# Performance work log

Measured on AMD Instinct MI355X. Metric: run time of the kernel, lower is better.

The kernel has to match this reference:

```python
import jax, jax.numpy as jnp
import numpy as np
import math

# Model hyperparameters (SchNet defaults)
H = 128        # hidden_channels
F = 128        # num_filters
G = 50         # num_gaussians
CUT = 6.0      # cutoff (Angstrom)
L_INT = 3      # num_interactions
# Graph scale
N_MOL = 512    # molecules
APM = 32       # atoms per molecule
N = N_MOL * APM
BOX = 10.0     # side of cubic box per molecule


def _ssp(x):
    # ShiftedSoftplus
    return jax.nn.softplus(x) - math.log(2.0)


def setup_inputs() -> dict:
    rng = np.random.default_rng(0)
    pos = rng.uniform(0.0, BOX, (N_MOL, APM, 3)).astype(np.float32)
    # radius graph within each molecule (faithful to radius_graph_custom,
    # precomputed here because edge count is data-dependent)
    srcs, dsts = [], []
    for m in range(N_MOL):
        p = pos[m]
        dm = np.linalg.norm(p[:, None, :] - p[None, :, :], axis=-1)
        mask = dm <= CUT
        np.fill_diagonal(mask, False)
        s, t = np.nonzero(mask)
        srcs.append(s + m * APM)
        dsts.append(t + m * APM)
    edge_index = np.stack([np.concatenate(srcs), np.concatenate(dsts)]).astype(np.int32)
    pos = pos.reshape(N, 3)
    batch = np.repeat(np.arange(N_MOL, dtype=np.int32), APM)
    z = rng.integers(1, 100, N).astype(np.int32)

    key = jax.random.key(0)
    ks = jax.random.split(key, 16)
    s = 0.1
    nrm = lambda k, shp: (jax.random.normal(k, shp, dtype=jnp.float32) * s)
    return {
        "z": jnp.asarray(z),
        "pos": jnp.asarray(pos),
        "batch": jnp.asarray(batch),
        "edge_index": jnp.asarray(edge_index),
        "emb": nrm(ks[0], (100, H)),
        "mlp_w1": nrm(ks[1], (L_INT, G, F)),
        "mlp_b1": jnp.zeros((L_INT, F), jnp.float32),
        "mlp_w2": nrm(ks[2], (L_INT, F, F)),
        "mlp_b2": jnp.zeros((L_INT, F), jnp.float32),
        "cf1_w": nrm(ks[3], (L_INT, H, F)),
        "cf2_w": nrm(ks[4], (L_INT, F, H)),
        "cf2_b": jnp.zeros((L_INT, H), jnp.float32),
        "lin_w": nrm(ks[5], (L_INT, H, H)),
        "lin_b": jnp.zeros((L_INT, H), jnp.float32),
        "out1_w": nrm(ks[6], (H, H // 2)),
        "out1_b": jnp.zeros((H // 2,), jnp.float32),
        "out2_w": nrm(ks[7], (H // 2, 1)),
        "out2_b": jnp.zeros((1,), jnp.float32),
    }


def reference(z, pos, batch, edge_index, emb,
              mlp_w1, mlp_b1, mlp_w2, mlp_b2,
              cf1_w, cf2_w, cf2_b, lin_w, lin_b,
              out1_w, out1_b, out2_w, out2_b):
    src, dst = edge_index[0], edge_index[1]
    # edge_weight = euclidean distance (== cdist[src, dst])
    d = jnp.sqrt(jnp.sum((pos[src] - pos[dst]) ** 2, axis=-1))  # [E]
    # GaussianSmearing
    offs = jnp.linspace(0.0, CUT, G)
    coeff = -0.5 / (CUT / (G - 1)) ** 2
    edge_attr = jnp.exp(coeff * (d[:, None] - offs[None, :]) ** 2)  # [E, G]
    # cosine cutoff
    Ccut = 0.5 * (jnp.cos(d * math.pi / CUT) + 1.0)  # [E]

    h = emb[z]  # [N, H]
    for l in range(L_INT):
        # edge filter MLP with cutoff
        W = _ssp(edge_attr @ mlp_w1[l] + mlp_b1[l]) @ mlp_w2[l] + mlp_b2[l]  # [E, F]
        W = W * Ccut[:, None]
        # CFConv: lin1 -> gather x_j -> multiply -> scatter-add to dst -> lin2
        msg = (h @ cf1_w[l])[src] * W                                # [E, F]
        agg = jax.ops.segment_sum(msg, dst, num_segments=N)          # [N, F]
        v = agg @ cf2_w[l] + cf2_b[l]                                # [N, H]
        v = _ssp(v)
        v = v @ lin_w[l] + lin_b[l]
        h = h + v  # residual

    h = _ssp(h @ out1_w + out1_b)
    h = h @ out2_w + out2_b                                          # [N, 1]
    out = jax.ops.segment_sum(h, batch, num_segments=N_MOL)          # [N_MOL, 1]
    return out
```

## Files before the change

kernel.cpp:

```cpp
#include <hip/hip_runtime.h>
#include <hip/hip_bf16.h>
#include <math.h>

#define NATOMS 16384
#define NMOL   512
#define APM    32
#define GDIM   50
#define KTAB   2048
#define MAXEPM 992

#define STRH 132
#define STRA 136

typedef __attribute__((ext_vector_type(8))) short   short8;
typedef __attribute__((ext_vector_type(4))) float   floatx4;

__device__ __forceinline__ float ssp(float x) {
    float e = __expf(-fabsf(x));
    return fmaxf(x, 0.0f) + __logf(1.0f + e) - 0.69314718055994531f;
}

__device__ __forceinline__ unsigned short f2bf(float x) {
    union { float f; unsigned int u; } v; v.f = x;
    unsigned int lsb = (v.u >> 16) & 1u;
    v.u += 0x7fffu + lsb;
    return (unsigned short)(v.u >> 16);
}

__device__ __forceinline__ unsigned int pk2bf(float a, float b) {
    __hip_bfloat162 h = __float22bfloat162_rn(make_float2(a, b));
    unsigned int u;
    __builtin_memcpy(&u, &h, 4);
    return u;
}

__global__ __launch_bounds__(256) void setup_kernel(
    const float* __restrict__ pos, const int* __restrict__ eidx, int E,
    int* __restrict__ rowptr,
    const float* __restrict__ cf1, const float* __restrict__ cf2,
    const float* __restrict__ lin, const float* __restrict__ out1,
    unsigned short* __restrict__ Wtall, uint2* __restrict__ meta)
{
    int idx = blockIdx.x * 256 + threadIdx.x;
    if (idx < E) {
        int s = eidx[idx], t = eidx[E + idx];
        float dx = pos[3 * s]     - pos[3 * t];
        float dy = pos[3 * s + 1] - pos[3 * t + 1];
        float dz = pos[3 * s + 2] - pos[3 * t + 2];
        float d  = sqrtf(dx * dx + dy * dy + dz * dz);
        float u  = d * (float)(KTAB - 1) / 6.0f;
        int i = min((int)u, KTAB - 2);
        float frac = u - (float)i;
        meta[idx] = make_uint2(((unsigned)i << 5) | (unsigned)(t & 31),
                               __float_as_uint(frac));
    } else if (idx < E + NATOMS + 1) {
        int a = idx - E;
        int lo = 0, hi = E;
        while (lo < hi) { int mid = (lo + hi) >> 1; if (eidx[mid] < a) lo = mid + 1; else hi = mid; }
        rowptr[a] = lo;
    } else if (idx < E + NATOMS + 1 + 9 * 16384 + 64 * 128) {
        int r = idx - (E + NATOMS + 1);
        if (r < 9 * 16384) {
            int wi = r >> 14, rem = r & 16383;
            int n = rem >> 7, k = rem & 127;
            int l = wi / 3, which = wi % 3;
            const float* src = (which == 0) ? cf1 : (which == 1) ? cf2 : lin;
            Wtall[r] = f2bf(src[(size_t)l * 16384 + k * 128 + n]);
        } else {
            int q = r - 9 * 16384;
            int n = q >> 7, k = q & 127;
            Wtall[r] = f2bf(out1[k * 64 + n]);
        }
    }
}

#define KW1 72
#define KW2 136

__global__ __launch_bounds__(256, 2) void build_table_kernel(
    const float* __restrict__ w1_, const float* __restrict__ b1_,
    const float* __restrict__ w2_, const float* __restrict__ b2_,
    unsigned short* __restrict__ T_)
{
    const int l = blockIdx.y;
    const float* w1 = w1_ + (size_t)l * GDIM * 128;
    const float* b1 = b1_ + (size_t)l * 128;
    const float* w2 = w2_ + (size_t)l * 128 * 128;
    const float* b2 = b2_ + (size_t)l * 128;
    unsigned short* T = T_ + (size_t)l * KTAB * 128;

    __shared__ unsigned short s_w1T[128 * KW1];
    __shared__ unsigned short s_w2T[128 * KW2];
    __shared__ unsigned short s_t[64 * KW2];

    const int tid = threadIdx.x;
    for (int i = tid; i < GDIM * 128; i += 256) {
        int g = i >> 7, f = i & 127;
        s_w1T[f * KW1 + g] = f2bf(w1[i]);
    }
    for (int i = tid; i < (64 - GDIM) * 128; i += 256) {
        int g = GDIM + (i >> 7), f = i & 127;
        s_w1T[f * KW1 + g] = 0;
    }
    for (int i = tid; i < 128 * 128; i += 256) {
        int k = i >> 7, n = i & 127;
        s_w2T[n * KW2 + k] = f2bf(w2[i]);
    }

    const int lane = tid & 63;
    const int w    = tid >> 6;
    const int l15  = lane & 15;
    const int quad = lane >> 4;

    float b1v[8], b2v[8];
    #pragma unroll
    for (int nt = 0; nt < 8; nt++) {
        b1v[nt] = b1[nt * 16 + l15];
        b2v[nt] = b2[nt * 16 + l15];
    }
    __syncthreads();

    const float hstep = 6.0f / (float)(KTAB - 1);
    const float step  = 6.0f / 49.0f;
    const float coeff = -0.5f / (step * step);
    const float pioc  = 3.14159265358979323846f / 6.0f;
    const int k0 = blockIdx.x * 64;
    const float dm = (float)(k0 + w * 16 + l15) * hstep;

    floatx4 acc1[8];
    #pragma unroll
    for (int nt = 0; nt < 8; nt++) acc1[nt] = (floatx4){0.f, 0.f, 0.f, 0.f};
    #pragma unroll
    for (int ks = 0; ks < 2; ks++) {
        unsigned int ap[4];
        #pragma unroll
        for (int jj = 0; jj < 4; jj++) {
            int g0 = ks * 32 + quad * 8 + 2 * jj;
            float d0 = dm - (float)g0 * step;
            float d1 = dm - (float)(g0 + 1) * step;
            float v0 = (g0 < GDIM)     ? __expf(coeff * d0 * d0) : 0.0f;
            float v1 = (g0 + 1 < GDIM) ? __expf(coeff * d1 * d1) : 0.0f;
            ap[jj] = pk2bf(v0, v1);
        }
        short8 af;
        __builtin_memcpy(&af, ap, 16);
        #pragma unroll
        for (int nt = 0; nt < 8; nt++) {
            short8 bfg = *(const short8*)&s_w1T[(nt * 16 + l15) * KW1 + ks * 32 + quad * 8];
            acc1[nt] = __builtin_amdgcn_mfma_f32_16x16x32_bf16(af, bfg, acc1[nt], 0, 0, 0);
        }
    }
    #pragma unroll
    for (int nt = 0; nt < 8; nt++) {
        #pragma unroll
        for (int r = 0; r < 4; r++) {
            int row = w * 16 + quad * 4 + r;
            s_t[row * KW2 + nt * 16 + l15] = f2bf(ssp(acc1[nt][r] + b1v[nt]));
        }
    }

    floatx4 acc2[8];
    #pragma unroll
    for (int nt = 0; nt < 8; nt++) acc2[nt] = (floatx4){0.f, 0.f, 0.f, 0.f};
    #pragma unroll
    for (int ks = 0; ks < 4; ks++) {
        short8 af = *(const short8*)&s_t[(w * 16 + l15) * KW2 + ks * 32 + quad * 8];
        #pragma unroll
        for (int nt = 0; nt < 8; nt++) {
            short8 bfg = *(const short8*)&s_w2T[(nt * 16 + l15) * KW2 + ks * 32 + quad * 8];
            acc2[nt] = __builtin_amdgcn_mfma_f32_16x16x32_bf16(af, bfg, acc2[nt], 0, 0, 0);
        }
    }

    #pragma unroll
    for (int nt = 0; nt < 8; nt++) {
        #pragma unroll
        for (int r = 0; r < 4; r++) {
            int row = w * 16 + quad * 4 + r;
            float d = (float)(k0 + row) * hstep;
            float cut = 0.5f * (__cosf(d * pioc) + 1.0f);
            T[(size_t)(k0 + row) * 128 + nt * 16 + l15] = f2bf((acc2[nt][r] + b2v[nt]) * cut);
        }
    }
}

__global__ __launch_bounds__(256) void pack_table_kernel(
    const unsigned short* __restrict__ T, unsigned int* __restrict__ Tp)
{
    int idx = blockIdx.x * 256 + threadIdx.x;
    int k = (idx >> 7) & (KTAB - 1);
    unsigned int w0 = T[idx];
    float w0f = __uint_as_float(w0 << 16);
    float w1f = (k == KTAB - 1) ? w0f
              : __uint_as_float((unsigned int)T[idx + 128] << 16);
    unsigned int dw = f2bf(w1f - w0f);
    Tp[idx] = w0 | (dw << 16);
}

__global__ __launch_bounds__(512) void fused_schnet_kernel(
    const int* __restrict__ z, const float* __restrict__ emb,
    const int* __restrict__ rowptr, const uint2* __restrict__ meta,
    const unsigned int* __restrict__ Tp,
    const unsigned short* __restrict__ Wtall,
    const float* __restrict__ cf2_b, const float* __restrict__ lin_b,
    const float* __restrict__ out1_b, const float* __restrict__ out2_w,
    const float* __restrict__ out2_b,
    float* __restrict__ out)
{
    __shared__ float s_h[32 * STRH];
    __shared__ float s_hx[32 * 128];
    __shared__ unsigned short s_agg[32 * STRA];
    __shared__ uint2 s_meta[MAXEPM];
    __shared__ float s_red;
    unsigned short* s_t = (unsigned short*)s_hx;

    const int tid  = threadIdx.x;
    const int lane = tid & 63;
    const int w    = tid >> 6;
    const int l15  = lane & 15;
    const int quad = lane >> 4;
    const int r16  = (w & 1) * 16;
    const int c32  = (w >> 1) * 32;
    const int B0   = blockIdx.x * 32;

    for (int i = tid; i < 32 * 128; i += 512) {
        int row = i >> 7, col = i & 127;
        s_h[row * STRH + col] = emb[(size_t)z[B0 + row] * 128 + col];
    }
    if (tid == 0) s_red = 0.0f;

    const int ebase = rowptr[B0];
    const int nE    = rowptr[B0 + 32] - ebase;
    for (int i = tid; i < nE; i += 512) s_meta[i] = meta[ebase + i];

    const int rp = rowptr[B0 + w * 4 + min(lane, 4)] - ebase;

    const unsigned short* WtO = Wtall + 9 * 16384;

    for (int l = 0; l < 3; l++) {
        const unsigned short* W1 = Wtall + (size_t)(l * 3 + 0) * 16384;
        const unsigned short* W2 = Wtall + (size_t)(l * 3 + 1) * 16384;
        const unsigned short* W3 = Wtall + (size_t)(l * 3 + 2) * 16384;
        const unsigned int* Tpl  = Tp + (size_t)l * KTAB * 128;

        __syncthreads();

        floatx4 acc[2];
        #pragma unroll
        for (int nt = 0; nt < 2; nt++) acc[nt] = (floatx4){0.f, 0.f, 0.f, 0.f};
        #pragma unroll
        for (int ks = 0; ks < 4; ks++) {
            const float* hp = &s_h[(r16 + l15) * STRH + ks * 32 + quad * 8];
            float4 xa = *(const float4*)hp;
            float4 xb = *(const float4*)(hp + 4);
            unsigned int ap[4];
            ap[0] = pk2bf(xa.x, xa.y); ap[1] = pk2bf(xa.z, xa.w);
            ap[2] = pk2bf(xb.x, xb.y); ap[3] = pk2bf(xb.z, xb.w);
            short8 af;
            __builtin_memcpy(&af, ap, 16);
            #pragma unroll
            for (int nt = 0; nt < 2; nt++) {
                short8 bfg = *(const short8*)&W1[(size_t)(c32 + nt * 16 + l15) * 128 + ks * 32 + quad * 8];
                acc[nt] = __builtin_amdgcn_mfma_f32_16x16x32_bf16(af, bfg, acc[nt], 0, 0, 0);
            }
        }
        #pragma unroll
        for (int nt = 0; nt < 2; nt++) {
            #pragma unroll
            for (int r = 0; r < 4; r++)
                s_hx[(r16 + quad * 4 + r) * 128 + c32 + nt * 16 + l15] = acc[nt][r];
        }

        __syncthreads();

        for (int al = 0; al < 4; al++) {
            const int e0 = __shfl(rp, al);
            const int e1 = __shfl(rp, al + 1);
            float ax[8], ay[8];
            #pragma unroll
            for (int j = 0; j < 8; j++) { ax[j] = 0.f; ay[j] = 0.f; }
            int e = e0;
            for (; e + 7 < e1; e += 8) {
                #pragma unroll
                for (int j = 0; j < 8; j++) {
                    uint2 q = s_meta[e + j];
                    int tl   = q.x & 31;
                    int knot = q.x >> 5;
                    uint2 tp = *(const uint2*)&Tpl[(size_t)knot * 128 + 2 * lane];
                    float2 hv = *(const float2*)&s_hx[tl * 128 + 2 * lane];
                    float fr = __uint_as_float(q.y);
                    float wx = fmaf(fr, __uint_as_float(tp.x & 0xffff0000u),
                                    __uint_as_float(tp.x << 16));
                    float wy = fmaf(fr, __uint_as_float(tp.y & 0xffff0000u),
                                    __uint_as_float(tp.y << 16));
                    ax[j] = fmaf(hv.x, wx, ax[j]);
                    ay[j] = fmaf(hv.y, wy, ay[j]);
                }
            }
            for (; e < e1; e++) {
                int j = (e - e0) & 7;
                uint2 q = s_meta[e];
                int tl   = q.x & 31;
                int knot = q.x >> 5;
                uint2 tp = *(const uint2*)&Tpl[(size_t)knot * 128 + 2 * lane];
                float2 hv = *(const float2*)&s_hx[tl * 128 + 2 * lane];
                float fr = __uint_as_float(q.y);
                float wx = fmaf(fr, __uint_as_float(tp.x & 0xffff0000u),
                                __uint_as_float(tp.x << 16));
                float wy = fmaf(fr, __uint_as_float(tp.y & 0xffff0000u),
                                __uint_as_float(tp.y << 16));
                ax[j] = fmaf(hv.x, wx, ax[j]);
                ay[j] = fmaf(hv.y, wy, ay[j]);
            }
            float sx = ((ax[0] + ax[1]) + (ax[2] + ax[3])) + ((ax[4] + ax[5]) + (ax[6] + ax[7]));
            float sy = ((ay[0] + ay[1]) + (ay[2] + ay[3])) + ((ay[4] + ay[5]) + (ay[6] + ay[7]));
            *(unsigned int*)&s_agg[(w * 4 + al) * STRA + 2 * lane] = pk2bf(sx, sy);
        }

        __syncthreads();

        float bva[2], bvb[2];
        #pragma unroll
        for (int nt = 0; nt < 2; nt++) {
            bva[nt] = cf2_b[l * 128 + c32 + nt * 16 + l15];
            bvb[nt] = lin_b[l * 128 + c32 + nt * 16 + l15];
        }
        #pragma unroll
        for (int nt = 0; nt < 2; nt++) acc[nt] = (floatx4){0.f, 0.f, 0.f, 0.f};
        #pragma unroll
        for (int ks = 0; ks < 4; ks++) {
            short8 af = *(const short8*)&s_agg[(r16 + l15) * STRA + ks * 32 + quad * 8];
            #pragma unroll
            for (int nt = 0; nt < 2; nt++) {
                short8 bfg = *(const short8*)&W2[(size_t)(c32 + nt * 16 + l15) * 128 + ks * 32 + quad * 8];
                acc[nt] = __builtin_amdgcn_mfma_f32_16x16x32_bf16(af, bfg, acc[nt], 0, 0, 0);
            }
        }
        #pragma unroll
        for (int nt = 0; nt < 2; nt++) {
            #pragma unroll
            for (int r = 0; r < 4; r++) {
                int row = r16 + quad * 4 + r;
                s_t[row * STRA + c32 + nt * 16 + l15] = f2bf(ssp(acc[nt][r] + bva[nt]));
            }
        }

        __syncthreads();

        #pragma unroll
        for (int nt = 0; nt < 2; nt++) acc[nt] = (floatx4){0.f, 0.f, 0.f, 0.f};
        #pragma unroll
        for (int ks = 0; ks < 4; ks++) {
            short8 af = *(const short8*)&s_t[(r16 + l15) * STRA + ks * 32 + quad * 8];
            #pragma unroll
            for (int nt = 0; nt < 2; nt++) {
                short8 bfg = *(const short8*)&W3[(size_t)(c32 + nt * 16 + l15) * 128 + ks * 32 + quad * 8];
                acc[nt] = __builtin_amdgcn_mfma_f32_16x16x32_bf16(af, bfg, acc[nt], 0, 0, 0);
            }
        }
        #pragma unroll
        for (int nt = 0; nt < 2; nt++) {
            #pragma unroll
            for (int r = 0; r < 4; r++) {
                int row = r16 + quad * 4 + r;
                s_h[row * STRH + c32 + nt * 16 + l15] += acc[nt][r] + bvb[nt];
            }
        }
    }

    __syncthreads();

    const int c16 = (w >> 1) * 16;
    floatx4 ha = (floatx4){0.f, 0.f, 0.f, 0.f};
    #pragma unroll
    for (int ks = 0; ks < 4; ks++) {
        const float* hp = &s_h[(r16 + l15) * STRH + ks * 32 + quad * 8];
        float4 xa = *(const float4*)hp;
        float4 xb = *(const float4*)(hp + 4);
        unsigned int ap[4];
        ap[0] = pk2bf(xa.x, xa.y); ap[1] = pk2bf(xa.z, xa.w);
        ap[2] = pk2bf(xb.x, xb.y); ap[3] = pk2bf(xb.z, xb.w);
        short8 af;
        __builtin_memcpy(&af, ap, 16);
        short8 bfg = *(const short8*)&WtO[(size_t)(c16 + l15) * 128 + ks * 32 + quad * 8];
        ha = __builtin_amdgcn_mfma_f32_16x16x32_bf16(af, bfg, ha, 0, 0, 0);
    }
    float part = 0.0f;
    {
        float b1o = out1_b[c16 + l15];
        float o2  = out2_w[c16 + l15];
        #pragma unroll
        for (int r = 0; r < 4; r++)
            part += ssp(ha[r] + b1o) * o2;
    }
    #pragma unroll
    for (int off = 32; off > 0; off >>= 1) part += __shfl_down(part, off);
    if (lane == 0) atomicAdd(&s_red, part);
    __syncthreads();
    if (tid == 0) out[blockIdx.x] = s_red + 32.0f * out2_b[0];
}

extern "C" void kernel_launch(void* const* d_in, const int* in_sizes, int n_in,
                              void* d_out, int out_size, void* d_ws, size_t ws_size,
                              hipStream_t stream)
{
    const int*   z      = (const int*)d_in[0];
    const float* pos    = (const float*)d_in[1];
    const int*   eidx   = (const int*)d_in[3];
    const float* emb    = (const float*)d_in[4];
    const float* mlp_w1 = (const float*)d_in[5];
    const float* mlp_b1 = (const float*)d_in[6];
    const float* mlp_w2 = (const float*)d_in[7];
    const float* mlp_b2 = (const float*)d_in[8];
    const float* cf1_w  = (const float*)d_in[9];
    const float* cf2_w  = (const float*)d_in[10];
    const float* cf2_b  = (const float*)d_in[11];
    const float* lin_w  = (const float*)d_in[12];
    const float* lin_b  = (const float*)d_in[13];
    const float* out1_w = (const float*)d_in[14];
    const float* out1_b = (const float*)d_in[15];
    const float* out2_w = (const float*)d_in[16];
    const float* out2_b = (const float*)d_in[17];
    const int E = in_sizes[3] / 2;

    char* p = (char*)d_ws;
    uint2* meta = (uint2*)p;                      p += ((size_t)E * 8 + 63) & ~63ULL;
    unsigned int* Tp = (unsigned int*)p;          p += (size_t)3 * KTAB * 128 * 4;
    int* rowptr = (int*)p;                        p += ((size_t)(NATOMS + 1) * 4 + 63) & ~63ULL;
    unsigned short* Ttab = (unsigned short*)p;    p += (size_t)3 * KTAB * 128 * 2;
    unsigned short* Wtall = (unsigned short*)p;

    const int setup_work = E + (NATOMS + 1) + 9 * 16384 + 64 * 128;
    setup_kernel<<<(setup_work + 255) / 256, 256, 0, stream>>>(
        pos, eidx, E, rowptr, cf1_w, cf2_w, lin_w, out1_w, Wtall, meta);
    build_table_kernel<<<dim3(KTAB / 64, 3), 256, 0, stream>>>(
        mlp_w1, mlp_b1, mlp_w2, mlp_b2, Ttab);
    pack_table_kernel<<<3 * KTAB * 128 / 256, 256, 0, stream>>>(Ttab, Tp);

    fused_schnet_kernel<<<NMOL, 512, 0, stream>>>(
        z, emb, rowptr, meta, Tp, Wtall,
        cf2_b, lin_b, out1_b, out2_w, out2_b, (float*)d_out);
}
```

Before: 187.4 us.

## Exploit edge symmetry: process each undirected edge once with LDS atomic scatter

Setup now keeps only edges with t > s, compacting them per molecule into a padded list with a ballot-based wave compaction, so the CSR rowptr build is no longer needed. The fused kernel processes each undirected pair once: one filter-table lookup serves both directions, and the result is scattered to both endpoint rows through LDS float atomics into an fp32 aggregate buffer. This halves the filter-table gathers and the interpolation work. In exchange it adds four shared-memory atomics per edge per lane, zeroes the aggregate buffer every layer, and converts it to bf16 before the MFMA. It also assumes the input graph is symmetric, which holds for a radius graph.

```diff
diff --git a/kernel.cpp b/kernel.cpp
--- a/kernel.cpp
+++ b/kernel.cpp
@@ -7,7 +7,7 @@
 #define APM    32
 #define GDIM   50
 #define KTAB   2048
-#define MAXEPM 992
+#define MAXU   512
 
 #define STRH 132
 #define STRA 136
@@ -36,41 +36,65 @@
 
 __global__ __launch_bounds__(256) void setup_kernel(
     const float* __restrict__ pos, const int* __restrict__ eidx, int E,
-    int* __restrict__ rowptr,
     const float* __restrict__ cf1, const float* __restrict__ cf2,
     const float* __restrict__ lin, const float* __restrict__ out1,
-    unsigned short* __restrict__ Wtall, uint2* __restrict__ meta)
+    unsigned short* __restrict__ Wtall, uint2* __restrict__ umeta,
+    int* __restrict__ ucnt)
 {
-    int idx = blockIdx.x * 256 + threadIdx.x;
-    if (idx < E) {
-        int s = eidx[idx], t = eidx[E + idx];
-        float dx = pos[3 * s]     - pos[3 * t];
-        float dy = pos[3 * s + 1] - pos[3 * t + 1];
-        float dz = pos[3 * s + 2] - pos[3 * t + 2];
-        float d  = sqrtf(dx * dx + dy * dy + dz * dz);
-        float u  = d * (float)(KTAB - 1) / 6.0f;
-        int i = min((int)u, KTAB - 2);
-        float frac = u - (float)i;
-        meta[idx] = make_uint2(((unsigned)i << 5) | (unsigned)(t & 31),
-                               __float_as_uint(frac));
-    } else if (idx < E + NATOMS + 1) {
-        int a = idx - E;
+    if (blockIdx.x < NMOL) {
+        const int lane = threadIdx.x;
+        if (lane >= 64) return;
+        const int m  = blockIdx.x;
+        const int B0 = m * 32;
         int lo = 0, hi = E;
-        while (lo < hi) { int mid = (lo + hi) >> 1; if (eidx[mid] < a) lo = mid + 1; else hi = mid; }
-        rowptr[a] = lo;
-    } else if (idx < E + NATOMS + 1 + 9 * 16384 + 64 * 128) {
-        int r = idx - (E + NATOMS + 1);
-        if (r < 9 * 16384) {
-            int wi = r >> 14, rem = r & 16383;
-            int n = rem >> 7, k = rem & 127;
-            int l = wi / 3, which = wi % 3;
-            const float* src = (which == 0) ? cf1 : (which == 1) ? cf2 : lin;
-            Wtall[r] = f2bf(src[(size_t)l * 16384 + k * 128 + n]);
-        } else {
-            int q = r - 9 * 16384;
-            int n = q >> 7, k = q & 127;
-            Wtall[r] = f2bf(out1[k * 64 + n]);
-        }
+        while (lo < hi) { int mid = (lo + hi) >> 1; if (eidx[mid] < B0) lo = mid + 1; else hi = mid; }
+        const int e0 = lo; hi = E;
+        while (lo < hi) { int mid = (lo + hi) >> 1; if (eidx[mid] < B0 + 32) lo = mid + 1; else hi = mid; }
+        const int e1 = lo;
+
+        uint2* out = umeta + (size_t)m * MAXU;
+        int cnt = 0;
+        for (int base = e0; base < e1; base += 64) {
+            int e = base + lane;
+            bool keep = false;
+            uint2 val;
+            if (e < e1) {
+                int s = eidx[e], t = eidx[E + e];
+                if (t > s) {
+                    float dx = pos[3 * s]     - pos[3 * t];
+                    float dy = pos[3 * s + 1] - pos[3 * t + 1];
+                    float dz = pos[3 * s + 2] - pos[3 * t + 2];
+                    float d  = sqrtf(dx * dx + dy * dy + dz * dz);
+                    float u  = d * (float)(KTAB - 1) / 6.0f;
+                    int i = min((int)u, KTAB - 2);
+                    val = make_uint2(((unsigned)i << 12) |
+                                     ((unsigned)(s - B0) << 6) | (unsigned)(t - B0),
+                                     __float_as_uint(u - (float)i));
+                    keep = true;
+                }
+            }
+            unsigned long long mask = __ballot(keep);
+            int slot = __popcll(mask & ((1ULL << lane) - 1ULL));
+            if (keep) out[cnt + slot] = val;
+            cnt += (int)__popcll(mask);
+        }
+        int padded = (cnt + 63) & ~63;
+        for (int e = cnt + lane; e < padded; e += 64)
+            out[e] = make_uint2((32u << 6) | 32u, 0u);
+        if (lane == 0) ucnt[m] = padded;
+        return;
+    }
+    int idx = (blockIdx.x - NMOL) * 256 + threadIdx.x;
+    if (idx < 9 * 16384) {
+        int wi = idx >> 14, rem = idx & 16383;
+        int n = rem >> 7, k = rem & 127;
+        int l = wi / 3, which = wi % 3;
+        const float* src = (which == 0) ? cf1 : (which == 1) ? cf2 : lin;
+        Wtall[idx] = f2bf(src[(size_t)l * 16384 + k * 128 + n]);
+    } else if (idx < 9 * 16384 + 64 * 128) {
+        int q = idx - 9 * 16384;
+        int n = q >> 7, k = q & 127;
+        Wtall[idx] = f2bf(out1[k * 64 + n]);
     }
 }
 
@@ -199,7 +223,7 @@
 
 __global__ __launch_bounds__(512) void fused_schnet_kernel(
     const int* __restrict__ z, const float* __restrict__ emb,
-    const int* __restrict__ rowptr, const uint2* __restrict__ meta,
+    const uint2* __restrict__ umeta, const int* __restrict__ ucnt,
     const unsigned int* __restrict__ Tp,
     const unsigned short* __restrict__ Wtall,
     const float* __restrict__ cf2_b, const float* __restrict__ lin_b,
@@ -208,12 +232,11 @@
     float* __restrict__ out)
 {
     __shared__ float s_h[32 * STRH];
-    __shared__ float s_hx[32 * 128];
-    __shared__ unsigned short s_agg[32 * STRA];
-    __shared__ uint2 s_meta[MAXEPM];
+    __shared__ float s_hx[33 * 128];
+    __shared__ float s_agg[33 * STRH];
+    __shared__ uint2 s_meta[MAXU];
     __shared__ float s_red;
     unsigned short* s_t = (unsigned short*)s_hx;
-
     const int tid  = threadIdx.x;
     const int lane = tid & 63;
     const int w    = tid >> 6;
@@ -227,13 +250,11 @@
         int row = i >> 7, col = i & 127;
         s_h[row * STRH + col] = emb[(size_t)z[B0 + row] * 128 + col];
     }
+    if (tid < 128) s_hx[32 * 128 + tid] = 0.0f;
     if (tid == 0) s_red = 0.0f;
 
-    const int ebase = rowptr[B0];
-    const int nE    = rowptr[B0 + 32] - ebase;
-    for (int i = tid; i < nE; i += 512) s_meta[i] = meta[ebase + i];
-
-    const int rp = rowptr[B0 + w * 4 + min(lane, 4)] - ebase;
+    const int nU = ucnt[blockIdx.x];
+    for (int i = tid; i < nU; i += 512) s_meta[i] = umeta[(size_t)blockIdx.x * MAXU + i];
 
     const unsigned short* WtO = Wtall + 9 * 16384;
 
@@ -244,6 +265,8 @@
         const unsigned int* Tpl  = Tp + (size_t)l * KTAB * 128;
 
         __syncthreads();
+
+        for (int i = tid; i < 32 * STRH; i += 512) s_agg[i] = 0.0f;
 
         floatx4 acc[2];
         #pragma unroll
@@ -273,48 +296,26 @@
 
         __syncthreads();
 
-        for (int al = 0; al < 4; al++) {
-            const int e0 = __shfl(rp, al);
-            const int e1 = __shfl(rp, al + 1);
-            float ax[8], ay[8];
-            #pragma unroll
-            for (int j = 0; j < 8; j++) { ax[j] = 0.f; ay[j] = 0.f; }
-            int e = e0;
-            for (; e + 7 < e1; e += 8) {
-                #pragma unroll
-                for (int j = 0; j < 8; j++) {
-                    uint2 q = s_meta[e + j];
-                    int tl   = q.x & 31;
-                    int knot = q.x >> 5;
-                    uint2 tp = *(const uint2*)&Tpl[(size_t)knot * 128 + 2 * lane];
-                    float2 hv = *(const float2*)&s_hx[tl * 128 + 2 * lane];
-                    float fr = __uint_as_float(q.y);
-                    float wx = fmaf(fr, __uint_as_float(tp.x & 0xffff0000u),
-                                    __uint_as_float(tp.x << 16));
-                    float wy = fmaf(fr, __uint_as_float(tp.y & 0xffff0000u),
-                                    __uint_as_float(tp.y << 16));
-                    ax[j] = fmaf(hv.x, wx, ax[j]);
-                    ay[j] = fmaf(hv.y, wy, ay[j]);
-                }
-            }
-            for (; e < e1; e++) {
-                int j = (e - e0) & 7;
-                uint2 q = s_meta[e];
-                int tl   = q.x & 31;
-                int knot = q.x >> 5;
+        for (int base = w * 8; base < nU; base += 64) {
+            #pragma unroll
+            for (int j = 0; j < 8; j++) {
+                uint2 q = s_meta[base + j];
+                int b    = q.x & 63;
+                int a    = (q.x >> 6) & 63;
+                int knot = q.x >> 12;
                 uint2 tp = *(const uint2*)&Tpl[(size_t)knot * 128 + 2 * lane];
-                float2 hv = *(const float2*)&s_hx[tl * 128 + 2 * lane];
+                float2 hva = *(const float2*)&s_hx[a * 128 + 2 * lane];
+                float2 hvb = *(const float2*)&s_hx[b * 128 + 2 * lane];
                 float fr = __uint_as_float(q.y);
                 float wx = fmaf(fr, __uint_as_float(tp.x & 0xffff0000u),
                                 __uint_as_float(tp.x << 16));
                 float wy = fmaf(fr, __uint_as_float(tp.y & 0xffff0000u),
                                 __uint_as_float(tp.y << 16));
-                ax[j] = fmaf(hv.x, wx, ax[j]);
-                ay[j] = fmaf(hv.y, wy, ay[j]);
-            }
-            float sx = ((ax[0] + ax[1]) + (ax[2] + ax[3])) + ((ax[4] + ax[5]) + (ax[6] + ax[7]));
-            float sy = ((ay[0] + ay[1]) + (ay[2] + ay[3])) + ((ay[4] + ay[5]) + (ay[6] + ay[7]));
-            *(unsigned int*)&s_agg[(w * 4 + al) * STRA + 2 * lane] = pk2bf(sx, sy);
+                atomicAdd(&s_agg[a * STRH + 2 * lane],     hvb.x * wx);
+                atomicAdd(&s_agg[a * STRH + 2 * lane + 1], hvb.y * wy);
+                atomicAdd(&s_agg[b * STRH + 2 * lane],     hva.x * wx);
+                atomicAdd(&s_agg[b * STRH + 2 * lane + 1], hva.y * wy);
+            }
         }
 
         __syncthreads();
@@ -329,7 +330,14 @@
         for (int nt = 0; nt < 2; nt++) acc[nt] = (floatx4){0.f, 0.f, 0.f, 0.f};
         #pragma unroll
         for (int ks = 0; ks < 4; ks++) {
-            short8 af = *(const short8*)&s_agg[(r16 + l15) * STRA + ks * 32 + quad * 8];
+            const float* apf = &s_agg[(r16 + l15) * STRH + ks * 32 + quad * 8];
+            float4 xa = *(const float4*)apf;
+            float4 xb = *(const float4*)(apf + 4);
+            unsigned int ap[4];
+            ap[0] = pk2bf(xa.x, xa.y); ap[1] = pk2bf(xa.z, xa.w);
+            ap[2] = pk2bf(xb.x, xb.y); ap[3] = pk2bf(xb.z, xb.w);
+            short8 af;
+            __builtin_memcpy(&af, ap, 16);
             #pragma unroll
             for (int nt = 0; nt < 2; nt++) {
                 short8 bfg = *(const short8*)&W2[(size_t)(c32 + nt * 16 + l15) * 128 + ks * 32 + quad * 8];
@@ -424,20 +432,20 @@
     const int E = in_sizes[3] / 2;
 
     char* p = (char*)d_ws;
-    uint2* meta = (uint2*)p;                      p += ((size_t)E * 8 + 63) & ~63ULL;
+    uint2* umeta = (uint2*)p;                     p += (size_t)NMOL * MAXU * 8;
     unsigned int* Tp = (unsigned int*)p;          p += (size_t)3 * KTAB * 128 * 4;
-    int* rowptr = (int*)p;                        p += ((size_t)(NATOMS + 1) * 4 + 63) & ~63ULL;
+    int* ucnt = (int*)p;                          p += ((size_t)NMOL * 4 + 63) & ~63ULL;
     unsigned short* Ttab = (unsigned short*)p;    p += (size_t)3 * KTAB * 128 * 2;
     unsigned short* Wtall = (unsigned short*)p;
 
-    const int setup_work = E + (NATOMS + 1) + 9 * 16384 + 64 * 128;
-    setup_kernel<<<(setup_work + 255) / 256, 256, 0, stream>>>(
-        pos, eidx, E, rowptr, cf1_w, cf2_w, lin_w, out1_w, Wtall, meta);
+    const int wblocks = (9 * 16384 + 64 * 128 + 255) / 256;
+    setup_kernel<<<NMOL + wblocks, 256, 0, stream>>>(
+        pos, eidx, E, cf1_w, cf2_w, lin_w, out1_w, Wtall, umeta, ucnt);
     build_table_kernel<<<dim3(KTAB / 64, 3), 256, 0, stream>>>(
         mlp_w1, mlp_b1, mlp_w2, mlp_b2, Ttab);
     pack_table_kernel<<<3 * KTAB * 128 / 256, 256, 0, stream>>>(Ttab, Tp);
 
     fused_schnet_kernel<<<NMOL, 512, 0, stream>>>(
-        z, emb, rowptr, meta, Tp, Wtall,
+        z, emb, umeta, ucnt, Tp, Wtall,
         cf2_b, lin_b, out1_b, out2_w, out2_b, (float*)d_out);
 }
```

New measurement: 710.7 us. +279.3%, slower.

## Merge setup, table build and pack into one kernel; widen edge gather loop

Applied to the files above, without the earlier changes.

The three preprocessing kernels (edge metadata and rowptr, weight conversion, filter-table build plus delta packing) are combined into one launch. The table build now emits packed value/delta pairs straight from LDS in overlapping 63-row tiles, which removes the intermediate bf16 table and the separate pack pass. In the main kernel the edge aggregation has each half-wave handle alternate edges with 4 channels per lane and 128-bit loads. The loop is padded with a sentinel edge that points at a zeroed h row, so the scalar tail loop goes away, and the two half-wave partials are combined with a cross-lane shuffle. This adds a 4-wave occupancy hint and some padded-edge work in return for fewer launches and wider memory accesses.

```diff
diff --git a/kernel.cpp b/kernel.cpp
--- a/kernel.cpp
+++ b/kernel.cpp
@@ -7,7 +7,7 @@
 #define APM    32
 #define GDIM   50
 #define KTAB   2048
-#define MAXEPM 992
+#define MAXEPM 1000
 
 #define STRH 132
 #define STRA 136
@@ -27,6 +27,11 @@
     return (unsigned short)(v.u >> 16);
 }
 
+__device__ __forceinline__ float bf2f(unsigned int u16bits) {
+    union { unsigned int u; float f; } v; v.u = u16bits << 16;
+    return v.f;
+}
+
 __device__ __forceinline__ unsigned int pk2bf(float a, float b) {
     __hip_bfloat162 h = __float22bfloat162_rn(make_float2(a, b));
     unsigned int u;
@@ -34,66 +39,78 @@
     return u;
 }
 
-__global__ __launch_bounds__(256) void setup_kernel(
-    const float* __restrict__ pos, const int* __restrict__ eidx, int E,
+#define KW1 72
+#define KW2 136
+#define TILE_K 63
+#define NTILE 33
+
+__global__ __launch_bounds__(256) void mega_setup_kernel(
+    const float* __restrict__ pos, const int* __restrict__ eidx, int E, int EB,
     int* __restrict__ rowptr,
     const float* __restrict__ cf1, const float* __restrict__ cf2,
     const float* __restrict__ lin, const float* __restrict__ out1,
-    unsigned short* __restrict__ Wtall, uint2* __restrict__ meta)
+    unsigned short* __restrict__ Wtall, uint2* __restrict__ meta,
+    const float* __restrict__ w1_, const float* __restrict__ b1_,
+    const float* __restrict__ w2_, const float* __restrict__ b2_,
+    unsigned int* __restrict__ Tp)
 {
-    int idx = blockIdx.x * 256 + threadIdx.x;
-    if (idx < E) {
-        int s = eidx[idx], t = eidx[E + idx];
-        float dx = pos[3 * s]     - pos[3 * t];
-        float dy = pos[3 * s + 1] - pos[3 * t + 1];
-        float dz = pos[3 * s + 2] - pos[3 * t + 2];
-        float d  = sqrtf(dx * dx + dy * dy + dz * dz);
-        float u  = d * (float)(KTAB - 1) / 6.0f;
-        int i = min((int)u, KTAB - 2);
-        float frac = u - (float)i;
-        meta[idx] = make_uint2(((unsigned)i << 5) | (unsigned)(t & 31),
-                               __float_as_uint(frac));
-    } else if (idx < E + NATOMS + 1) {
-        int a = idx - E;
-        int lo = 0, hi = E;
-        while (lo < hi) { int mid = (lo + hi) >> 1; if (eidx[mid] < a) lo = mid + 1; else hi = mid; }
-        rowptr[a] = lo;
-    } else if (idx < E + NATOMS + 1 + 9 * 16384 + 64 * 128) {
-        int r = idx - (E + NATOMS + 1);
-        if (r < 9 * 16384) {
-            int wi = r >> 14, rem = r & 16383;
+    const int WB = (9 * 16384 + 64 * 128 + 255) / 256;
+    const int b = blockIdx.x;
+    const int tid = threadIdx.x;
+
+    if (b < EB) {
+        int idx = b * 256 + tid;
+        if (idx < E) {
+            int s = eidx[idx], t = eidx[E + idx];
+            float dx = pos[3 * s]     - pos[3 * t];
+            float dy = pos[3 * s + 1] - pos[3 * t + 1];
+            float dz = pos[3 * s + 2] - pos[3 * t + 2];
+            float d  = sqrtf(dx * dx + dy * dy + dz * dz);
+            float u  = d * (float)(KTAB - 1) / 6.0f;
+            int i = min((int)u, KTAB - 2);
+            meta[idx] = make_uint2(((unsigned)i << 6) | (unsigned)(t & 31),
+                                   __float_as_uint(u - (float)i));
+        } else if (idx < E + NATOMS + 1) {
+            int a = idx - E;
+            if (a == 0) meta[E] = make_uint2(32u, 0u);
+            int lo = 0, hi = E;
+            while (lo < hi) { int mid = (lo + hi) >> 1; if (eidx[mid] < a) lo = mid + 1; else hi = mid; }
+            rowptr[a] = lo;
+        }
+        return;
+    }
+    if (b < EB + WB) {
+        int idx = (b - EB) * 256 + tid;
+        if (idx < 9 * 16384) {
+            int wi = idx >> 14, rem = idx & 16383;
             int n = rem >> 7, k = rem & 127;
             int l = wi / 3, which = wi % 3;
             const float* src = (which == 0) ? cf1 : (which == 1) ? cf2 : lin;
-            Wtall[r] = f2bf(src[(size_t)l * 16384 + k * 128 + n]);
-        } else {
-            int q = r - 9 * 16384;
+            Wtall[idx] = f2bf(src[(size_t)l * 16384 + k * 128 + n]);
+        } else if (idx < 9 * 16384 + 64 * 128) {
+            int q = idx - 9 * 16384;
             int n = q >> 7, k = q & 127;
-            Wtall[r] = f2bf(out1[k * 64 + n]);
-        }
-    }
-}
-
-#define KW1 72
-#define KW2 136
-
-__global__ __launch_bounds__(256, 2) void build_table_kernel(
-    const float* __restrict__ w1_, const float* __restrict__ b1_,
-    const float* __restrict__ w2_, const float* __restrict__ b2_,
-    unsigned short* __restrict__ T_)
-{
-    const int l = blockIdx.y;
+            Wtall[idx] = f2bf(out1[k * 64 + n]);
+        }
+        return;
+    }
+
+    __shared__ unsigned short s_bufA[128 * KW2];
+    __shared__ unsigned short s_bufB[128 * KW1];
+
+    const int tt = b - EB - WB;
+    const int l  = tt / NTILE;
+    const int bx = tt % NTILE;
     const float* w1 = w1_ + (size_t)l * GDIM * 128;
     const float* b1 = b1_ + (size_t)l * 128;
     const float* w2 = w2_ + (size_t)l * 128 * 128;
     const float* b2 = b2_ + (size_t)l * 128;
-    unsigned short* T = T_ + (size_t)l * KTAB * 128;
-
-    __shared__ unsigned short s_w1T[128 * KW1];
-    __shared__ unsigned short s_w2T[128 * KW2];
-    __shared__ unsigned short s_t[64 * KW2];
-
-    const int tid = threadIdx.x;
+    unsigned int* Tpg = Tp + (size_t)l * KTAB * 128;
+
+    unsigned short* s_w1T = s_bufB;
+    unsigned short* s_w2T = s_bufA;
+    unsigned short* s_t   = s_bufB;
+
     for (int i = tid; i < GDIM * 128; i += 256) {
         int g = i >> 7, f = i & 127;
         s_w1T[f * KW1 + g] = f2bf(w1[i]);
@@ -124,7 +141,7 @@
     const float step  = 6.0f / 49.0f;
     const float coeff = -0.5f / (step * step);
     const float pioc  = 3.14159265358979323846f / 6.0f;
-    const int k0 = blockIdx.x * 64;
+    const int k0 = bx * TILE_K;
     const float dm = (float)(k0 + w * 16 + l15) * hstep;
 
     floatx4 acc1[8];
@@ -150,6 +167,8 @@
             acc1[nt] = __builtin_amdgcn_mfma_f32_16x16x32_bf16(af, bfg, acc1[nt], 0, 0, 0);
         }
     }
+    __syncthreads();
+
     #pragma unroll
     for (int nt = 0; nt < 8; nt++) {
         #pragma unroll
@@ -172,6 +191,7 @@
         }
     }
 
+    unsigned short* T_lds = s_t;
     #pragma unroll
     for (int nt = 0; nt < 8; nt++) {
         #pragma unroll
@@ -179,25 +199,24 @@
             int row = w * 16 + quad * 4 + r;
             float d = (float)(k0 + row) * hstep;
             float cut = 0.5f * (__cosf(d * pioc) + 1.0f);
-            T[(size_t)(k0 + row) * 128 + nt * 16 + l15] = f2bf((acc2[nt][r] + b2v[nt]) * cut);
-        }
-    }
-}
-
-__global__ __launch_bounds__(256) void pack_table_kernel(
-    const unsigned short* __restrict__ T, unsigned int* __restrict__ Tp)
-{
-    int idx = blockIdx.x * 256 + threadIdx.x;
-    int k = (idx >> 7) & (KTAB - 1);
-    unsigned int w0 = T[idx];
-    float w0f = __uint_as_float(w0 << 16);
-    float w1f = (k == KTAB - 1) ? w0f
-              : __uint_as_float((unsigned int)T[idx + 128] << 16);
-    unsigned int dw = f2bf(w1f - w0f);
-    Tp[idx] = w0 | (dw << 16);
-}
-
-__global__ __launch_bounds__(512) void fused_schnet_kernel(
+            T_lds[row * KW2 + nt * 16 + l15] = f2bf((acc2[nt][r] + b2v[nt]) * cut);
+        }
+    }
+    __syncthreads();
+
+    for (int i = tid; i < TILE_K * 128; i += 256) {
+        int r = i >> 7, f = i & 127;
+        int k = k0 + r;
+        if (k <= KTAB - 2) {
+            unsigned int w0 = T_lds[r * KW2 + f];
+            unsigned int w1b = T_lds[(r + 1) * KW2 + f];
+            unsigned int dw = f2bf(bf2f(w1b) - bf2f(w0));
+            Tpg[(size_t)k * 128 + f] = w0 | (dw << 16);
+        }
+    }
+}
+
+__global__ __launch_bounds__(512, 4) void fused_schnet_kernel(
     const int* __restrict__ z, const float* __restrict__ emb,
     const int* __restrict__ rowptr, const uint2* __restrict__ meta,
     const unsigned int* __restrict__ Tp,
@@ -208,7 +227,7 @@
     float* __restrict__ out)
 {
     __shared__ float s_h[32 * STRH];
-    __shared__ float s_hx[32 * 128];
+    __shared__ float s_hx[33 * 128];
     __shared__ unsigned short s_agg[32 * STRA];
     __shared__ uint2 s_meta[MAXEPM];
     __shared__ float s_red;
@@ -221,17 +240,21 @@
     const int quad = lane >> 4;
     const int r16  = (w & 1) * 16;
     const int c32  = (w >> 1) * 32;
+    const int pair = lane >> 5;
+    const int c4   = (lane & 31) * 4;
     const int B0   = blockIdx.x * 32;
 
     for (int i = tid; i < 32 * 128; i += 512) {
         int row = i >> 7, col = i & 127;
         s_h[row * STRH + col] = emb[(size_t)z[B0 + row] * 128 + col];
     }
+    if (tid < 128) s_hx[32 * 128 + tid] = 0.0f;
     if (tid == 0) s_red = 0.0f;
 
     const int ebase = rowptr[B0];
     const int nE    = rowptr[B0 + 32] - ebase;
     for (int i = tid; i < nE; i += 512) s_meta[i] = meta[ebase + i];
+    if (tid == 0) s_meta[nE] = make_uint2(32u, 0u);
 
     const int rp = rowptr[B0 + w * 4 + min(lane, 4)] - ebase;
 
@@ -276,45 +299,42 @@
         for (int al = 0; al < 4; al++) {
             const int e0 = __shfl(rp, al);
             const int e1 = __shfl(rp, al + 1);
-            float ax[8], ay[8];
-            #pragma unroll
-            for (int j = 0; j < 8; j++) { ax[j] = 0.f; ay[j] = 0.f; }
-            int e = e0;
-            for (; e + 7 < e1; e += 8) {
+            float a0[8], a1[8], a2[8], a3[8];
+            #pragma unroll
+            for (int j = 0; j < 8; j++) { a0[j] = a1[j] = a2[j] = a3[j] = 0.f; }
+            for (int e = e0; e < e1; e += 16) {
                 #pragma unroll
                 for (int j = 0; j < 8; j++) {
-                    uint2 q = s_meta[e + j];
-                    int tl   = q.x & 31;
-                    int knot = q.x >> 5;
-                    uint2 tp = *(const uint2*)&Tpl[(size_t)knot * 128 + 2 * lane];
-                    float2 hv = *(const float2*)&s_hx[tl * 128 + 2 * lane];
+                    int idx = e + 2 * j + pair;
+                    idx = (idx < e1) ? idx : nE;
+                    uint2 q = s_meta[idx];
+                    int tl   = q.x & 63;
+                    int knot = q.x >> 6;
+                    uint4 tp = *(const uint4*)&Tpl[(size_t)knot * 128 + c4];
+                    float4 hv = *(const float4*)&s_hx[tl * 128 + c4];
                     float fr = __uint_as_float(q.y);
-                    float wx = fmaf(fr, __uint_as_float(tp.x & 0xffff0000u),
-                                    __uint_as_float(tp.x << 16));
-                    float wy = fmaf(fr, __uint_as_float(tp.y & 0xffff0000u),
-                                    __uint_as_float(tp.y << 16));
-                    ax[j] = fmaf(hv.x, wx, ax[j]);
-                    ay[j] = fmaf(hv.y, wy, ay[j]);
+                    a0[j] = fmaf(hv.x, fmaf(fr, __uint_as_float(tp.x & 0xffff0000u),
+                                            __uint_as_float(tp.x << 16)), a0[j]);
+                    a1[j] = fmaf(hv.y, fmaf(fr, __uint_as_float(tp.y & 0xffff0000u),
+                                            __uint_as_float(tp.y << 16)), a1[j]);
+                    a2[j] = fmaf(hv.z, fmaf(fr, __uint_as_float(tp.z & 0xffff0000u),
+                                            __uint_as_float(tp.z << 16)), a2[j]);
+                    a3[j] = fmaf(hv.w, fmaf(fr, __uint_as_float(tp.w & 0xffff0000u),
+                                            __uint_as_float(tp.w << 16)), a3[j]);
                 }
             }
-            for (; e < e1; e++) {
-                int j = (e - e0) & 7;
-                uint2 q = s_meta[e];
-                int tl   = q.x & 31;
-                int knot = q.x >> 5;
-                uint2 tp = *(const uint2*)&Tpl[(size_t)knot * 128 + 2 * lane];
-                float2 hv = *(const float2*)&s_hx[tl * 128 + 2 * lane];
-                float fr = __uint_as_float(q.y);
-                float wx = fmaf(fr, __uint_as_float(tp.x & 0xffff0000u),
-                                __uint_as_float(tp.x << 16));
-                float wy = fmaf(fr, __uint_as_float(tp.y & 0xffff0000u),
-                                __uint_as_float(tp.y << 16));
-                ax[j] = fmaf(hv.x, wx, ax[j]);
-                ay[j] = fmaf(hv.y, wy, ay[j]);
-            }
-            float sx = ((ax[0] + ax[1]) + (ax[2] + ax[3])) + ((ax[4] + ax[5]) + (ax[6] + ax[7]));
-            float sy = ((ay[0] + ay[1]) + (ay[2] + ay[3])) + ((ay[4] + ay[5]) + (ay[6] + ay[7]));
-            *(unsigned int*)&s_agg[(w * 4 + al) * STRA + 2 * lane] = pk2bf(sx, sy);
+            float s0 = ((a0[0] + a0[1]) + (a0[2] + a0[3])) + ((a0[4] + a0[5]) + (a0[6] + a0[7]));
+            float s1 = ((a1[0] + a1[1]) + (a1[2] + a1[3])) + ((a1[4] + a1[5]) + (a1[6] + a1[7]));
+            float s2 = ((a2[0] + a2[1]) + (a2[2] + a2[3])) + ((a2[4] + a2[5]) + (a2[6] + a2[7]));
+            float s3 = ((a3[0] + a3[1]) + (a3[2] + a3[3])) + ((a3[4] + a3[5]) + (a3[6] + a3[7]));
+            s0 += __shfl_xor(s0, 32);
+            s1 += __shfl_xor(s1, 32);
+            s2 += __shfl_xor(s2, 32);
+            s3 += __shfl_xor(s3, 32);
+            if (pair == 0) {
+                uint2 pkd = make_uint2(pk2bf(s0, s1), pk2bf(s2, s3));
+                *(uint2*)&s_agg[(w * 4 + al) * STRA + c4] = pkd;
+            }
         }
 
         __syncthreads();
@@ -424,18 +444,17 @@
     const int E = in_sizes[3] / 2;
 
     char* p = (char*)d_ws;
-    uint2* meta = (uint2*)p;                      p += ((size_t)E * 8 + 63) & ~63ULL;
+    uint2* meta = (uint2*)p;                      p += ((size_t)(E + 1) * 8 + 63) & ~63ULL;
     unsigned int* Tp = (unsigned int*)p;          p += (size_t)3 * KTAB * 128 * 4;
     int* rowptr = (int*)p;                        p += ((size_t)(NATOMS + 1) * 4 + 63) & ~63ULL;
-    unsigned short* Ttab = (unsigned short*)p;    p += (size_t)3 * KTAB * 128 * 2;
     unsigned short* Wtall = (unsigned short*)p;
 
-    const int setup_work = E + (NATOMS + 1) + 9 * 16384 + 64 * 128;
-    setup_kernel<<<(setup_work + 255) / 256, 256, 0, stream>>>(
-        pos, eidx, E, rowptr, cf1_w, cf2_w, lin_w, out1_w, Wtall, meta);
-    build_table_kernel<<<dim3(KTAB / 64, 3), 256, 0, stream>>>(
-        mlp_w1, mlp_b1, mlp_w2, mlp_b2, Ttab);
-    pack_table_kernel<<<3 * KTAB * 128 / 256, 256, 0, stream>>>(Ttab, Tp);
+    const int EB = (E + NATOMS + 1 + 255) / 256;
+    const int WB = (9 * 16384 + 64 * 128 + 255) / 256;
+    const int TB = NTILE * 3;
+    mega_setup_kernel<<<EB + WB + TB, 256, 0, stream>>>(
+        pos, eidx, E, EB, rowptr, cf1_w, cf2_w, lin_w, out1_w, Wtall, meta,
+        mlp_w1, mlp_b1, mlp_w2, mlp_b2, Tp);
 
     fused_schnet_kernel<<<NMOL, 512, 0, stream>>>(
         z, emb, rowptr, meta, Tp, Wtall,
```

New measurement: 180.7 us. -3.6%, faster.
